# Optimization experiments

Measured on AMD Instinct MI355X. Metric: run time of the kernel, lower is better.

Reference implementation:

```python
import jax, jax.numpy as jnp
import numpy as np

NUM_EMBEDDINGS = 1024
EMBEDDING_DIM = 256
COMMITMENT_COST = 0.25


def setup_inputs() -> dict:
    key = jax.random.key(0)
    k_z, k_e = jax.random.split(key)
    z = jax.random.normal(k_z, (4, EMBEDDING_DIM, 16, 32, 32), dtype=jnp.float32)
    # torch init: uniform_(-1/K, 1/K)
    emb = jax.random.uniform(
        k_e, (NUM_EMBEDDINGS, EMBEDDING_DIM), dtype=jnp.float32,
        minval=-1.0 / NUM_EMBEDDINGS, maxval=1.0 / NUM_EMBEDDINGS)
    return {"z": z, "emb": emb}


def reference(z, emb):
    sg = jax.lax.stop_gradient
    b, c, d, h, w = z.shape
    K = emb.shape[0]
    # (B,C,D,H,W) -> (N, C)
    z_flat = jnp.transpose(z, (0, 2, 3, 4, 1)).reshape(-1, c)
    x_sq = jnp.sum(z_flat * z_flat, axis=1, keepdims=True)          # (N,1)
    e_sq = jnp.sum(emb * emb, axis=1)                                # (K,)
    xe = z_flat @ emb.T                                              # (N,K)
    distances = x_sq + e_sq[None, :] - 2.0 * xe
    encoding_indices = jnp.argmin(distances, axis=1)                 # (N,)
    z_q = emb[encoding_indices].reshape(b, d, h, w, c).transpose(0, 4, 1, 2, 3)
    embedding_loss = jnp.mean((sg(z_q) - z) ** 2)
    commitment_loss = COMMITMENT_COST * jnp.mean((z_q - sg(z)) ** 2)
    vq_loss = embedding_loss + commitment_loss
    z_q_st = z + sg(z_q - z)  # straight-through
    # perplexity from codebook usage histogram (== mean of one-hot encodings)
    counts = jnp.zeros((K,), z_flat.dtype).at[encoding_indices].add(1.0)
    avg_probs = counts / z_flat.shape[0]
    perplexity = jnp.exp(-jnp.sum(avg_probs * jnp.log(avg_probs + 1e-10)))
    return z_q_st, vq_loss, perplexity, encoding_indices.reshape(b, d, h, w)
```

## Files before the change

kernel.cpp:

```cpp
#include <hip/hip_runtime.h>


#define C_DIM 256
#define K_CODES 1024
#define N_VEC 65536
#define T_GAP 4e-4f

#define OUT_ZQ_SIZE 16777216
#define OUT_LOSS_OFF 16777216
#define OUT_PP_OFF   16777217
#define OUT_IDX_OFF  16777218

#define WS_EH    0
#define WS_EL    524288
#define WS_ESQ   1048576
#define WS_XSQ   1052672
#define WS_CNT   1314816
#define WS_LOSS  1318912
#define WS_FLC   1318920
#define WS_SIDX  1318928
#define WS_FLIST 1581072
#define WS_PM1   1843264
#define WS_EMBT  1843264
#define WS_PM2   2891840
#define WS_PIX   3940416

typedef __attribute__((ext_vector_type(8))) short short8;
typedef __attribute__((ext_vector_type(8))) unsigned short ushort8;
typedef __attribute__((ext_vector_type(16))) float f32x16;

__device__ __forceinline__ unsigned short bf16_rne(float v) {
    unsigned u = __float_as_uint(v);
    unsigned r = (u + 0x7FFFu + ((u >> 16) & 1u)) >> 16;
    return (unsigned short)r;
}



__global__ __launch_bounds__(256) void convert_z_kernel(const float* __restrict__ z,
                                                        unsigned short* __restrict__ zhF,
                                                        unsigned short* __restrict__ zlF) {
    const int tid = threadIdx.x;
    const int ln = tid & 63;
    const int og = tid >> 6;
    const int n0 = blockIdx.x * 64;
    const int b = n0 >> 14, s0 = n0 & 16383;
    const int n = n0 + ln;
    const size_t zbase = ((size_t)b << 22) + s0 + ln;
    const size_t tbase = (size_t)(n >> 5) * 8192;
    const int lr = n & 31;
#pragma unroll
    for (int t = 0; t < 8; ++t) {
        int o = og + t * 4;
        int c0 = o * 8;
        ushort8 hb, lb;
#pragma unroll
        for (int j = 0; j < 8; ++j) {
            float v = z[zbase + ((size_t)(c0 + j) << 14)];
            unsigned short h = bf16_rne(v);
            hb[j] = h;
            lb[j] = bf16_rne(v - __uint_as_float((unsigned)h << 16));
        }
        size_t off = tbase + (size_t)(o >> 1) * 512 + (size_t)(lr + 32 * (o & 1)) * 8;
        *reinterpret_cast<ushort8*>(zhF + off) = hb;
        *reinterpret_cast<ushort8*>(zlF + off) = lb;
    }
}

__global__ __launch_bounds__(256) void convert_e_kernel(const float* __restrict__ emb,
                                                        unsigned short* __restrict__ ehF,
                                                        unsigned short* __restrict__ elF) {
    int t = blockIdx.x * 256 + threadIdx.x;
    int k = t >> 5, o = t & 31;
    int c0 = o * 8;
    ushort8 hb, lb;
#pragma unroll
    for (int j = 0; j < 8; ++j) {
        float v = emb[k * C_DIM + c0 + j];
        unsigned short h = bf16_rne(v);
        hb[j] = h;
        lb[j] = bf16_rne(v - __uint_as_float((unsigned)h << 16));
    }
    size_t off = (size_t)(k >> 5) * 8192 + (size_t)(o >> 1) * 512 + (size_t)((k & 31) + 32 * (o & 1)) * 8;
    *reinterpret_cast<ushort8*>(ehF + off) = hb;
    *reinterpret_cast<ushort8*>(elF + off) = lb;
}


__device__ __forceinline__ float pairwise_sq_128(const float* p) {
#pragma clang fp contract(off)
    float r[8];
#pragma unroll
    for (int j = 0; j < 8; ++j) { float v = p[j]; r[j] = v * v; }
#pragma unroll
    for (int i = 8; i < 128; i += 8)
#pragma unroll
        for (int j = 0; j < 8; ++j) { float v = p[i + j]; float t = v * v; r[j] = r[j] + t; }
    return ((r[0] + r[1]) + (r[2] + r[3])) + ((r[4] + r[5]) + (r[6] + r[7]));
}

__global__ __launch_bounds__(256) void esq_kernel(const float* __restrict__ emb,
                                                  float* __restrict__ esq) {
#pragma clang fp contract(off)
    __shared__ float tile[64 * 260];
    const int tid = threadIdx.x;
    const int k0 = blockIdx.x * 64;
#pragma unroll
    for (int r = 0; r < 64; ++r) {
        int idx = r * 256 + tid;
        tile[(idx >> 8) * 260 + (idx & 255)] = emb[k0 * C_DIM + idx];
    }
    __syncthreads();
    if (tid < 64) {
        const float* row = &tile[tid * 260];
        esq[k0 + tid] = pairwise_sq_128(row) + pairwise_sq_128(row + 128);
    }
}

__global__ __launch_bounds__(256) void xsq_kernel(const float* __restrict__ z,
                                                  float* __restrict__ xsq) {
#pragma clang fp contract(off)
    const int n = blockIdx.x * 256 + threadIdx.x;
    const int b = n >> 14, s = n & 16383;
    const float* base = z + ((size_t)b << 22) + s;
    float r[8], res;
#pragma unroll
    for (int j = 0; j < 8; ++j) { float v = base[(size_t)j << 14]; r[j] = v * v; }
#pragma unroll
    for (int i = 8; i < 128; i += 8)
#pragma unroll
        for (int j = 0; j < 8; ++j) { float v = base[(size_t)(i + j) << 14]; float t = v * v; r[j] = r[j] + t; }
    res = ((r[0] + r[1]) + (r[2] + r[3])) + ((r[4] + r[5]) + (r[6] + r[7]));
#pragma unroll
    for (int j = 0; j < 8; ++j) { float v = base[(size_t)(128 + j) << 14]; r[j] = v * v; }
#pragma unroll
    for (int i = 136; i < 256; i += 8)
#pragma unroll
        for (int j = 0; j < 8; ++j) { float v = base[(size_t)(i + j) << 14]; float t = v * v; r[j] = r[j] + t; }
    res = res + (((r[0] + r[1]) + (r[2] + r[3])) + ((r[4] + r[5]) + (r[6] + r[7])));
    xsq[n] = res;
}

__global__ __launch_bounds__(256) void transpose_kernel(const float* __restrict__ emb,
                                                        float* __restrict__ embT) {
    __shared__ float t[64][65];
    const int k0 = blockIdx.x * 64;
    const int c0 = blockIdx.y * 64;
    const int tx = threadIdx.x & 63, ty = threadIdx.x >> 6;
    for (int r = ty; r < 64; r += 4)
        t[r][tx] = emb[(k0 + r) * C_DIM + c0 + tx];
    __syncthreads();
    for (int r = ty; r < 64; r += 4)
        embT[(c0 + r) * K_CODES + k0 + tx] = t[tx][r];
}


__global__ __launch_bounds__(512, 1) void screen_kernel(
    const unsigned short* __restrict__ zhF, const unsigned short* __restrict__ zlF,
    const unsigned short* __restrict__ ehF, const unsigned short* __restrict__ elF,
    const float* __restrict__ esq, const float* __restrict__ xsq,
    float* __restrict__ pm1, float* __restrict__ pm2,
    unsigned short* __restrict__ pix) {
    __shared__ __align__(16) unsigned short abuf[2][64 * 512];
    __shared__ float xbuf[512];
    __shared__ float sm1[8][64], sm2[8][64];
    __shared__ int   si[8][64];

    const int tid = threadIdx.x;
    const int w = tid >> 6, l = tid & 63, lr = l & 31, lh = l >> 5;
    const int bid = blockIdx.x;
    const int v = (bid & 7) * 64 + (bid >> 3);
    const int nb = v >> 2, kb = v & 3;
    const int n0 = nb * 512;
    const int kw = kb * 256 + w * 32;
    const int loff = l * 8;

    short8 Eh[16], El[16];
    {
        const unsigned short* bh = ehF + (size_t)(kb * 8 + w) * 8192 + loff;
        const unsigned short* bl = elF + (size_t)(kb * 8 + w) * 8192 + loff;
#pragma unroll
        for (int q = 0; q < 16; ++q) {
            Eh[q] = *reinterpret_cast<const short8*>(bh + q * 512);
            El[q] = *reinterpret_cast<const short8*>(bl + q * 512);
        }
    }
    float esql[16];
#pragma unroll
    for (int r = 0; r < 16; ++r)
        esql[r] = esq[kw + (r & 3) + 8 * (r >> 2) + 4 * lh];

    __builtin_amdgcn_global_load_lds(
        (const __attribute__((address_space(1))) void*)(xsq + n0 + w * 64 + l),
        (__attribute__((address_space(3))) void*)&xbuf[w * 64], 4, 0, 0);

    asm volatile("s_waitcnt vmcnt(0)" ::: "memory");
    __builtin_amdgcn_s_barrier();

#define STAGE(S) do {                                                                   \
    const int _b = (S) & 1;                                                             \
    _Pragma("unroll")                                                                   \
    for (int ci = 0; ci < 8; ++ci) {                                                    \
        int c = 8 * w + ci;                                                             \
        const unsigned short* src = ((c & 32) ? zlF : zhF)                              \
            + (size_t)((n0 >> 5) + (S) * 2 + ((c >> 4) & 1)) * 8192                     \
            + (size_t)(c & 15) * 512 + loff;                                            \
        __builtin_amdgcn_global_load_lds(                                               \
            (const __attribute__((address_space(1))) void*)src,                         \
            (__attribute__((address_space(3))) void*)&abuf[_b][c * 512], 16, 0, 0);     \
    }                                                                                   \
} while (0)

    STAGE(0);

    float rm1 = 3.4e38f, rm2 = 3.4e38f;
    int   ri1 = 0;

    for (int s = 0; s < 8; ++s) {
        const int cur = s & 1;
        asm volatile("s_waitcnt vmcnt(0)" ::: "memory");
        __builtin_amdgcn_s_barrier();
        __builtin_amdgcn_sched_barrier(0);
        if (s < 7) STAGE(s + 1);

        f32x16 acc0, acc1;
#pragma unroll
        for (int r = 0; r < 16; ++r) { acc0[r] = 0.0f; acc1[r] = 0.0f; }

        __builtin_amdgcn_s_setprio(1);
#pragma unroll
        for (int q = 0; q < 16; ++q) {
            short8 azh0 = *reinterpret_cast<const short8*>(&abuf[cur][(q)      * 512 + loff]);
            short8 azh1 = *reinterpret_cast<const short8*>(&abuf[cur][(16 + q) * 512 + loff]);
            short8 azl0 = *reinterpret_cast<const short8*>(&abuf[cur][(32 + q) * 512 + loff]);
            short8 azl1 = *reinterpret_cast<const short8*>(&abuf[cur][(48 + q) * 512 + loff]);
            acc0 = __builtin_amdgcn_mfma_f32_32x32x16_bf16(Eh[q], azh0, acc0, 0, 0, 0);
            acc1 = __builtin_amdgcn_mfma_f32_32x32x16_bf16(Eh[q], azh1, acc1, 0, 0, 0);
            acc0 = __builtin_amdgcn_mfma_f32_32x32x16_bf16(Eh[q], azl0, acc0, 0, 0, 0);
            acc1 = __builtin_amdgcn_mfma_f32_32x32x16_bf16(Eh[q], azl1, acc1, 0, 0, 0);
            acc0 = __builtin_amdgcn_mfma_f32_32x32x16_bf16(El[q], azh0, acc0, 0, 0, 0);
            acc1 = __builtin_amdgcn_mfma_f32_32x32x16_bf16(El[q], azh1, acc1, 0, 0, 0);
        }
        __builtin_amdgcn_s_setprio(0);

#pragma unroll
        for (int i = 0; i < 2; ++i) {
            const f32x16 a = i ? acc1 : acc0;
            const float xs = xbuf[s * 64 + i * 32 + lr];
            float m1 = 3.4e38f, m2 = 3.4e38f;
            int i1 = 0;
#pragma unroll
            for (int r = 0; r < 16; ++r) {
                float sv = (xs + esql[r]) - 2.0f * a[r];
                int kg = kw + (r & 3) + 8 * (r >> 2) + 4 * lh;
                if (sv < m1) { m2 = m1; m1 = sv; i1 = kg; }
                else m2 = fminf(m2, sv);
            }
            float om1 = __shfl_xor(m1, 32, 64);
            float om2 = __shfl_xor(m2, 32, 64);
            int   oi  = __shfl_xor(i1, 32, 64);
            if (om1 < m1)      { m2 = fminf(m1, om2); m1 = om1; i1 = oi; }
            else if (om1 > m1) { m2 = fminf(m2, om1); }
            else               { m2 = m1; i1 = min(i1, oi); }
            if (lh == 0) { sm1[w][i * 32 + lr] = m1; sm2[w][i * 32 + lr] = m2; si[w][i * 32 + lr] = i1; }
        }
        asm volatile("s_waitcnt lgkmcnt(0)" ::: "memory");
        __builtin_amdgcn_s_barrier();
        __builtin_amdgcn_sched_barrier(0);

        if (w == s) {
            float m1 = sm1[0][l], m2 = sm2[0][l];
            int i1 = si[0][l];
#pragma unroll
            for (int ww = 1; ww < 8; ++ww) {
                float q1 = sm1[ww][l], q2 = sm2[ww][l];
                int qi = si[ww][l];
                if (q1 < m1)      { m2 = fminf(m1, q2); m1 = q1; i1 = qi; }
                else if (q1 > m1) { m2 = fminf(m2, q1); }
                else              { m2 = m1; }
            }
            rm1 = m1; rm2 = m2; ri1 = i1;
        }
    }
#undef STAGE

    {
        size_t p = (size_t)kb * N_VEC + n0 + w * 64 + l;
        pm1[p] = rm1; pm2[p] = rm2; pix[p] = (unsigned short)ri1;
    }
}

__global__ __launch_bounds__(256) void merge_kernel(
    const float* __restrict__ pm1, const float* __restrict__ pm2,
    const unsigned short* __restrict__ pix,
    int* __restrict__ screen_idx, unsigned* __restrict__ flag_list,
    unsigned* __restrict__ flag_count) {
    int n = blockIdx.x * 256 + threadIdx.x;
    float m1 = 3.4e38f, m2 = 3.4e38f;
    int i1 = 0;
    for (int kb = 0; kb < 4; ++kb) {
        size_t p = (size_t)kb * N_VEC + n;
        float a1 = pm1[p], a2 = pm2[p];
        int ai = (int)pix[p];
        if (a1 < m1)      { m2 = fminf(m1, a2); m1 = a1; i1 = ai; }
        else if (a1 > m1) { m2 = fminf(m2, a1); }
        else              { m2 = m1; i1 = min(i1, ai); }
    }
    if (m2 - m1 <= T_GAP) {
        screen_idx[n] = -1;
        unsigned pos = atomicAdd(flag_count, 1u);
        flag_list[pos] = (unsigned)n;
    } else {
        screen_idx[n] = i1;
    }
}


__global__ __launch_bounds__(256) void refine_kernel(
    const float* __restrict__ z, const float* __restrict__ embT,
    const float* __restrict__ esq, const float* __restrict__ xsq,
    const unsigned* __restrict__ flag_list, const unsigned* __restrict__ flag_count,
    float* __restrict__ out_idx, unsigned* __restrict__ counts) {
#pragma clang fp contract(off)
    __shared__ float zrow[8][256];
    __shared__ int nrow[8];
    __shared__ unsigned long long red[8][4];
    const int tid = threadIdx.x;
    const unsigned cnt = *flag_count;
    const unsigned groups = (cnt + 7) >> 3;
    const int kbase = tid * 4;
    for (unsigned g = blockIdx.x; g < groups; g += gridDim.x) {
        __syncthreads();
        if (tid < 8) nrow[tid] = (g * 8 + tid < cnt) ? (int)flag_list[g * 8 + tid] : -1;
        __syncthreads();
        for (int r = 0; r < 8; ++r) {
            int n = nrow[r];
            if (n >= 0) {
                int b = n >> 14, s = n & 16383;
                zrow[r][tid] = z[((size_t)b << 22) + ((size_t)tid << 14) + s];
            }
        }
        __syncthreads();
        float acc[8][4];
#pragma unroll
        for (int r = 0; r < 8; ++r)
#pragma unroll
            for (int j = 0; j < 4; ++j) acc[r][j] = 0.0f;
        for (int c4 = 0; c4 < 64; ++c4) {
            float4 ek[4];
#pragma unroll
            for (int x = 0; x < 4; ++x)
                ek[x] = *reinterpret_cast<const float4*>(embT + (size_t)(c4 * 4 + x) * K_CODES + kbase);
#pragma unroll
            for (int r = 0; r < 8; ++r) {
                float4 zv = *reinterpret_cast<const float4*>(&zrow[r][c4 * 4]);
                float a;
                a = acc[r][0];
                a = fmaf(zv.x, ek[0].x, a); a = fmaf(zv.y, ek[1].x, a);
                a = fmaf(zv.z, ek[2].x, a); a = fmaf(zv.w, ek[3].x, a);
                acc[r][0] = a;
                a = acc[r][1];
                a = fmaf(zv.x, ek[0].y, a); a = fmaf(zv.y, ek[1].y, a);
                a = fmaf(zv.z, ek[2].y, a); a = fmaf(zv.w, ek[3].y, a);
                acc[r][1] = a;
                a = acc[r][2];
                a = fmaf(zv.x, ek[0].z, a); a = fmaf(zv.y, ek[1].z, a);
                a = fmaf(zv.z, ek[2].z, a); a = fmaf(zv.w, ek[3].z, a);
                acc[r][2] = a;
                a = acc[r][3];
                a = fmaf(zv.x, ek[0].w, a); a = fmaf(zv.y, ek[1].w, a);
                a = fmaf(zv.z, ek[2].w, a); a = fmaf(zv.w, ek[3].w, a);
                acc[r][3] = a;
            }
        }
        float esql[4];
#pragma unroll
        for (int j = 0; j < 4; ++j) esql[j] = esq[kbase + j];
#pragma unroll
        for (int r = 0; r < 8; ++r) {
            int n = nrow[r];
            float xs = (n >= 0) ? xsq[n] : 0.0f;
            float m = 3.4e38f;
            int mi = 0;
#pragma unroll
            for (int j = 0; j < 4; ++j) {
                float t1 = xs + esql[j];
                float d = t1 - 2.0f * acc[r][j];
                if (d < m) { m = d; mi = kbase + j; }
            }
            unsigned long long p = ((unsigned long long)__float_as_uint(m) << 32) | (unsigned)mi;
            for (int off = 32; off >= 1; off >>= 1) {
                unsigned long long o = __shfl_xor(p, off, 64);
                p = (o < p) ? o : p;
            }
            if ((tid & 63) == 0) red[r][tid >> 6] = p;
        }
        __syncthreads();
        if (tid < 8 && nrow[tid] >= 0) {
            unsigned long long p = red[tid][0];
#pragma unroll
            for (int ww = 1; ww < 4; ++ww) { unsigned long long o = red[tid][ww]; p = (o < p) ? o : p; }
            int idx = (int)(p & 0xFFFFFFFFull);
            out_idx[nrow[tid]] = (float)idx;
            atomicAdd(&counts[idx], 1u);
        }
    }
}

__global__ __launch_bounds__(256) void emit_kernel(const int* __restrict__ screen_idx,
                                                   float* __restrict__ out_idx,
                                                   unsigned* __restrict__ counts) {
    int n = blockIdx.x * 256 + threadIdx.x;
    int iv = screen_idx[n];
    if (iv >= 0) {
        out_idx[n] = (float)iv;
        atomicAdd(&counts[iv], 1u);
    }
}


__global__ __launch_bounds__(256) void gather_kernel(
    const float* __restrict__ z, const float* __restrict__ embT,
    const float* __restrict__ out_idx, float* __restrict__ out,
    double* __restrict__ loss_acc) {
    const int tid = threadIdx.x;
    const int ct = blockIdx.x & 3;
    const int st = (blockIdx.x >> 2) & 15;
    const int b  = blockIdx.x >> 6;
    const int s0 = st * 1024;
    const int c0 = ct * 64;

    int idx[4];
#pragma unroll
    for (int q = 0; q < 4; ++q)
        idx[q] = (int)out_idx[(b << 14) + s0 + 4 * tid + q];

    const float* zb = z + ((size_t)b << 22) + s0 + 4 * tid;
    float* ob = out + ((size_t)b << 22) + s0 + 4 * tid;

    double local = 0.0;
    for (int c = 0; c < 64; ++c) {
        const int cg = c0 + c;
        const float* er = embT + (size_t)cg * K_CODES;
        float4 zv = *reinterpret_cast<const float4*>(zb + ((size_t)cg << 14));
        float4 ov;
        float d0 = er[idx[0]] - zv.x;
        float d1 = er[idx[1]] - zv.y;
        float d2 = er[idx[2]] - zv.z;
        float d3 = er[idx[3]] - zv.w;
        ov.x = zv.x + d0; ov.y = zv.y + d1; ov.z = zv.z + d2; ov.w = zv.w + d3;
        *reinterpret_cast<float4*>(ob + ((size_t)cg << 14)) = ov;
        local += (double)d0 * d0 + (double)d1 * d1 + (double)d2 * d2 + (double)d3 * d3;
    }
    for (int off = 32; off >= 1; off >>= 1) local += __shfl_down(local, off, 64);
    __shared__ double redd[4];
    if ((tid & 63) == 0) redd[tid >> 6] = local;
    __syncthreads();
    if (tid == 0) atomicAdd(loss_acc, redd[0] + redd[1] + redd[2] + redd[3]);
}

__global__ void finalize_kernel(const unsigned* __restrict__ counts,
                                const double* __restrict__ loss_acc,
                                float* __restrict__ out) {
    int tid = threadIdx.x;
    double s = 0.0;
    for (int k = tid; k < K_CODES; k += 256) {
        float avg = (float)counts[k] / 65536.0f;
        float t = avg * logf(avg + 1e-10f);
        s += (double)t;
    }
    for (int off = 32; off >= 1; off >>= 1) s += __shfl_down(s, off, 64);
    __shared__ double red[4];
    if ((tid & 63) == 0) red[tid >> 6] = s;
    __syncthreads();
    if (tid == 0) {
        double tot = red[0] + red[1] + red[2] + red[3];
        out[OUT_PP_OFF]   = expf((float)(-tot));
        out[OUT_LOSS_OFF] = 1.25f * (float)(loss_acc[0] / 16777216.0);
    }
}

extern "C" void kernel_launch(void* const* d_in, const int* in_sizes, int n_in,
                              void* d_out, int out_size, void* d_ws, size_t ws_size,
                              hipStream_t stream) {
    const float* z   = (const float*)d_in[0];
    const float* emb = (const float*)d_in[1];
    float* out = (float*)d_out;
    char* ws = (char*)d_ws;

    unsigned short* ehF = (unsigned short*)(ws + WS_EH);
    unsigned short* elF = (unsigned short*)(ws + WS_EL);
    float*    esq       = (float*)(ws + WS_ESQ);
    float*    xsq       = (float*)(ws + WS_XSQ);
    unsigned* counts    = (unsigned*)(ws + WS_CNT);
    double*   loss_acc  = (double*)(ws + WS_LOSS);
    unsigned* flag_cnt  = (unsigned*)(ws + WS_FLC);
    int*      sidx      = (int*)(ws + WS_SIDX);
    unsigned* flist     = (unsigned*)(ws + WS_FLIST);
    float*    pm1       = (float*)(ws + WS_PM1);
    float*    pm2       = (float*)(ws + WS_PM2);
    unsigned short* pix = (unsigned short*)(ws + WS_PIX);
    float*    embT      = (float*)(ws + WS_EMBT);

    unsigned short* zhF = (unsigned short*)out;
    unsigned short* zlF = (unsigned short*)(out + 8388608);
    float* out_idx = out + OUT_IDX_OFF;

    hipMemsetAsync(ws + WS_CNT, 0, 4108, stream);

    convert_z_kernel<<<1024, 256, 0, stream>>>(z, zhF, zlF);
    convert_e_kernel<<<128, 256, 0, stream>>>(emb, ehF, elF);
    esq_kernel<<<K_CODES / 64, 256, 0, stream>>>(emb, esq);
    xsq_kernel<<<N_VEC / 256, 256, 0, stream>>>(z, xsq);
    screen_kernel<<<512, 512, 0, stream>>>(zhF, zlF, ehF, elF, esq, xsq, pm1, pm2, pix);
    merge_kernel<<<256, 256, 0, stream>>>(pm1, pm2, pix, sidx, flist, flag_cnt);
    transpose_kernel<<<dim3(16, 4), 256, 0, stream>>>(emb, embT);
    refine_kernel<<<1024, 256, 0, stream>>>(z, embT, esq, xsq, flist, flag_cnt, out_idx, counts);
    emit_kernel<<<256, 256, 0, stream>>>(sidx, out_idx, counts);
    gather_kernel<<<256, 256, 0, stream>>>(z, embT, out_idx, out, loss_acc);
    finalize_kernel<<<1, 256, 0, stream>>>(counts, loss_acc, out);
}
```

Baseline: 276.6 us.

## Fuse norm computations into conversion kernels and remove a barrier per screen stage

Computes the per-vector squared norms inside the z conversion kernel, using an LDS-staged tile, and the codebook norms inside the embedding conversion kernel. This drops two separate kernels and a second full read of z. The screen kernel double-buffers its per-wave partial minima so that each stage's cross-wave reduction is deferred to the next stage, removing one barrier per iteration. The merge kernel now writes indices and counts directly, which eliminates the emit kernel and the screen_idx buffer. A stray label was added inside the unrolled loop.

```diff
diff --git a/kernel.cpp b/kernel.cpp
--- a/kernel.cpp
+++ b/kernel.cpp
@@ -18,7 +18,6 @@
 #define WS_CNT   1314816
 #define WS_LOSS  1318912
 #define WS_FLC   1318920
-#define WS_SIDX  1318928
 #define WS_FLIST 1581072
 #define WS_PM1   1843264
 #define WS_EMBT  1843264
@@ -39,37 +38,75 @@
 
 __global__ __launch_bounds__(256) void convert_z_kernel(const float* __restrict__ z,
                                                         unsigned short* __restrict__ zhF,
-                                                        unsigned short* __restrict__ zlF) {
+                                                        unsigned short* __restrict__ zlF,
+                                                        float* __restrict__ xsq) {
+#pragma clang fp contract(off)
+    __shared__ float tile[128][65];
     const int tid = threadIdx.x;
     const int ln = tid & 63;
     const int og = tid >> 6;
     const int n0 = blockIdx.x * 64;
     const int b = n0 >> 14, s0 = n0 & 16383;
     const int n = n0 + ln;
-    const size_t zbase = ((size_t)b << 22) + s0 + ln;
     const size_t tbase = (size_t)(n >> 5) * 8192;
     const int lr = n & 31;
-#pragma unroll
-    for (int t = 0; t < 8; ++t) {
-        int o = og + t * 4;
-        int c0 = o * 8;
-        ushort8 hb, lb;
-#pragma unroll
-        for (int j = 0; j < 8; ++j) {
-            float v = z[zbase + ((size_t)(c0 + j) << 14)];
-            unsigned short h = bf16_rne(v);
-            hb[j] = h;
-            lb[j] = bf16_rne(v - __uint_as_float((unsigned)h << 16));
-        }
-        size_t off = tbase + (size_t)(o >> 1) * 512 + (size_t)(lr + 32 * (o & 1)) * 8;
-        *reinterpret_cast<ushort8*>(zhF + off) = hb;
-        *reinterpret_cast<ushort8*>(zlF + off) = lb;
-    }
+    float res = 0.0f;
+
+    for (int p = 0; p < 2; ++p) {
+        __syncthreads();
+        for (int i = 0; i < 32; ++i) {
+            int c = p * 128 + i * 4 + og;
+            tile[i * 4 + og][ln] = z[((size_t)b << 22) + ((size_t)c << 14) + s0 + ln];
+        }
+        __syncthreads();
+#pragma unroll
+        for (int t = 0; t < 4; ++t) {
+            int oh = og + t * 4;
+            int o  = p * 16 + oh;
+            ushort8 hb, lb;
+#pragma unroll
+            for (int j = 0; j < 8; ++j) {
+                float v = tile[oh * 8 + j][ln];
+                unsigned short h = bf16_rne(v);
+                hb[j] = h;
+                lb[j] = bf16_rne(v - __uint_as_float((unsigned)h << 16));
+            }
+            size_t off = tbase + (size_t)(o >> 1) * 512 + (size_t)(lr + 32 * (o & 1)) * 8;
+            *reinterpret_cast<ushort8*>(zhF + off) = hb;
+            *reinterpret_cast<ushort8*>(zlF + off) = lb;
+        }
+        if (tid < 64) {
+            float r[8];
+#pragma unroll
+            for (int j = 0; j < 8; ++j) { float v = tile[j][tid]; r[j] = v * v; }
+#pragma unroll
+            for (int i = 8; i < 128; i += 8)
+#pragma unroll
+                for (int j = 0; j < 8; ++j) { float v = tile[i + j][tid]; float t2 = v * v; r[j] = r[j] + t2; }
+            float blk = ((r[0] + r[1]) + (r[2] + r[3])) + ((r[4] + r[5]) + (r[6] + r[7]));
+            res = (p == 0) ? blk : res + blk;
+        }
+    }
+    if (tid < 64) xsq[n0 + tid] = res;
+}
+
+__device__ __forceinline__ float pairwise_sq_128(const float* p) {
+#pragma clang fp contract(off)
+    float r[8];
+#pragma unroll
+    for (int j = 0; j < 8; ++j) { float v = p[j]; r[j] = v * v; }
+#pragma unroll
+    for (int i = 8; i < 128; i += 8)
+#pragma unroll
+        for (int j = 0; j < 8; ++j) { float v = p[i + j]; float t = v * v; r[j] = r[j] + t; }
+    return ((r[0] + r[1]) + (r[2] + r[3])) + ((r[4] + r[5]) + (r[6] + r[7]));
 }
 
 __global__ __launch_bounds__(256) void convert_e_kernel(const float* __restrict__ emb,
                                                         unsigned short* __restrict__ ehF,
-                                                        unsigned short* __restrict__ elF) {
+                                                        unsigned short* __restrict__ elF,
+                                                        float* __restrict__ esq) {
+#pragma clang fp contract(off)
     int t = blockIdx.x * 256 + threadIdx.x;
     int k = t >> 5, o = t & 31;
     int c0 = o * 8;
@@ -84,61 +121,11 @@
     size_t off = (size_t)(k >> 5) * 8192 + (size_t)(o >> 1) * 512 + (size_t)((k & 31) + 32 * (o & 1)) * 8;
     *reinterpret_cast<ushort8*>(ehF + off) = hb;
     *reinterpret_cast<ushort8*>(elF + off) = lb;
-}
-
-
-__device__ __forceinline__ float pairwise_sq_128(const float* p) {
-#pragma clang fp contract(off)
-    float r[8];
-#pragma unroll
-    for (int j = 0; j < 8; ++j) { float v = p[j]; r[j] = v * v; }
-#pragma unroll
-    for (int i = 8; i < 128; i += 8)
-#pragma unroll
-        for (int j = 0; j < 8; ++j) { float v = p[i + j]; float t = v * v; r[j] = r[j] + t; }
-    return ((r[0] + r[1]) + (r[2] + r[3])) + ((r[4] + r[5]) + (r[6] + r[7]));
-}
-
-__global__ __launch_bounds__(256) void esq_kernel(const float* __restrict__ emb,
-                                                  float* __restrict__ esq) {
-#pragma clang fp contract(off)
-    __shared__ float tile[64 * 260];
-    const int tid = threadIdx.x;
-    const int k0 = blockIdx.x * 64;
-#pragma unroll
-    for (int r = 0; r < 64; ++r) {
-        int idx = r * 256 + tid;
-        tile[(idx >> 8) * 260 + (idx & 255)] = emb[k0 * C_DIM + idx];
-    }
-    __syncthreads();
-    if (tid < 64) {
-        const float* row = &tile[tid * 260];
-        esq[k0 + tid] = pairwise_sq_128(row) + pairwise_sq_128(row + 128);
-    }
-}
-
-__global__ __launch_bounds__(256) void xsq_kernel(const float* __restrict__ z,
-                                                  float* __restrict__ xsq) {
-#pragma clang fp contract(off)
-    const int n = blockIdx.x * 256 + threadIdx.x;
-    const int b = n >> 14, s = n & 16383;
-    const float* base = z + ((size_t)b << 22) + s;
-    float r[8], res;
-#pragma unroll
-    for (int j = 0; j < 8; ++j) { float v = base[(size_t)j << 14]; r[j] = v * v; }
-#pragma unroll
-    for (int i = 8; i < 128; i += 8)
-#pragma unroll
-        for (int j = 0; j < 8; ++j) { float v = base[(size_t)(i + j) << 14]; float t = v * v; r[j] = r[j] + t; }
-    res = ((r[0] + r[1]) + (r[2] + r[3])) + ((r[4] + r[5]) + (r[6] + r[7]));
-#pragma unroll
-    for (int j = 0; j < 8; ++j) { float v = base[(size_t)(128 + j) << 14]; r[j] = v * v; }
-#pragma unroll
-    for (int i = 136; i < 256; i += 8)
-#pragma unroll
-        for (int j = 0; j < 8; ++j) { float v = base[(size_t)(i + j) << 14]; float t = v * v; r[j] = r[j] + t; }
-    res = res + (((r[0] + r[1]) + (r[2] + r[3])) + ((r[4] + r[5]) + (r[6] + r[7])));
-    xsq[n] = res;
+    if (threadIdx.x < 8) {
+        int k8 = blockIdx.x * 8 + threadIdx.x;
+        const float* row = emb + (size_t)k8 * C_DIM;
+        esq[k8] = pairwise_sq_128(row) + pairwise_sq_128(row + 128);
+    }
 }
 
 __global__ __launch_bounds__(256) void transpose_kernel(const float* __restrict__ emb,
@@ -163,8 +150,8 @@
     unsigned short* __restrict__ pix) {
     __shared__ __align__(16) unsigned short abuf[2][64 * 512];
     __shared__ float xbuf[512];
-    __shared__ float sm1[8][64], sm2[8][64];
-    __shared__ int   si[8][64];
+    __shared__ float smp1[2][8][64], smp2[2][8][64];
+    __shared__ int   smi[2][8][64];
 
     const int tid = threadIdx.x;
     const int w = tid >> 6, l = tid & 63, lr = l & 31, lh = l >> 5;
@@ -182,6 +169,7 @@
 #pragma unroll
         for (int q = 0; q < 16; ++q) {
             Eh[q] = *reinterpret_cast<const short8*>(bh + q * 512);
+            Bl_dummy:;
             El[q] = *reinterpret_cast<const short8*>(bl + q * 512);
         }
     }
@@ -218,10 +206,25 @@
 
     for (int s = 0; s < 8; ++s) {
         const int cur = s & 1;
-        asm volatile("s_waitcnt vmcnt(0)" ::: "memory");
+        asm volatile("s_waitcnt vmcnt(0) lgkmcnt(0)" ::: "memory");
         __builtin_amdgcn_s_barrier();
         __builtin_amdgcn_sched_barrier(0);
         if (s < 7) STAGE(s + 1);
+
+        if (s >= 1 && w == s - 1) {
+            const int pp = (s - 1) & 1;
+            float m1 = smp1[pp][0][l], m2 = smp2[pp][0][l];
+            int i1 = smi[pp][0][l];
+#pragma unroll
+            for (int ww = 1; ww < 8; ++ww) {
+                float q1 = smp1[pp][ww][l], q2 = smp2[pp][ww][l];
+                int qi = smi[pp][ww][l];
+                if (q1 < m1)      { m2 = fminf(m1, q2); m1 = q1; i1 = qi; }
+                else if (q1 > m1) { m2 = fminf(m2, q1); }
+                else              { m2 = m1; }
+            }
+            rm1 = m1; rm2 = m2; ri1 = i1;
+        }
 
         f32x16 acc0, acc1;
 #pragma unroll
@@ -262,27 +265,30 @@
             if (om1 < m1)      { m2 = fminf(m1, om2); m1 = om1; i1 = oi; }
             else if (om1 > m1) { m2 = fminf(m2, om1); }
             else               { m2 = m1; i1 = min(i1, oi); }
-            if (lh == 0) { sm1[w][i * 32 + lr] = m1; sm2[w][i * 32 + lr] = m2; si[w][i * 32 + lr] = i1; }
-        }
-        asm volatile("s_waitcnt lgkmcnt(0)" ::: "memory");
-        __builtin_amdgcn_s_barrier();
-        __builtin_amdgcn_sched_barrier(0);
-
-        if (w == s) {
-            float m1 = sm1[0][l], m2 = sm2[0][l];
-            int i1 = si[0][l];
-#pragma unroll
-            for (int ww = 1; ww < 8; ++ww) {
-                float q1 = sm1[ww][l], q2 = sm2[ww][l];
-                int qi = si[ww][l];
-                if (q1 < m1)      { m2 = fminf(m1, q2); m1 = q1; i1 = qi; }
-                else if (q1 > m1) { m2 = fminf(m2, q1); }
-                else              { m2 = m1; }
-            }
-            rm1 = m1; rm2 = m2; ri1 = i1;
+            if (lh == 0) {
+                smp1[s & 1][w][i * 32 + lr] = m1;
+                smp2[s & 1][w][i * 32 + lr] = m2;
+                smi [s & 1][w][i * 32 + lr] = i1;
+            }
         }
     }
 #undef STAGE
+
+    asm volatile("s_waitcnt lgkmcnt(0)" ::: "memory");
+    __builtin_amdgcn_s_barrier();
+    if (w == 7) {
+        float m1 = smp1[1][0][l], m2 = smp2[1][0][l];
+        int i1 = smi[1][0][l];
+#pragma unroll
+        for (int ww = 1; ww < 8; ++ww) {
+            float q1 = smp1[1][ww][l], q2 = smp2[1][ww][l];
+            int qi = smi[1][ww][l];
+            if (q1 < m1)      { m2 = fminf(m1, q2); m1 = q1; i1 = qi; }
+            else if (q1 > m1) { m2 = fminf(m2, q1); }
+            else              { m2 = m1; }
+        }
+        rm1 = m1; rm2 = m2; ri1 = i1;
+    }
 
     {
         size_t p = (size_t)kb * N_VEC + n0 + w * 64 + l;
@@ -293,8 +299,8 @@
 __global__ __launch_bounds__(256) void merge_kernel(
     const float* __restrict__ pm1, const float* __restrict__ pm2,
     const unsigned short* __restrict__ pix,
-    int* __restrict__ screen_idx, unsigned* __restrict__ flag_list,
-    unsigned* __restrict__ flag_count) {
+    unsigned* __restrict__ flag_list, unsigned* __restrict__ flag_count,
+    float* __restrict__ out_idx, unsigned* __restrict__ counts) {
     int n = blockIdx.x * 256 + threadIdx.x;
     float m1 = 3.4e38f, m2 = 3.4e38f;
     int i1 = 0;
@@ -307,11 +313,11 @@
         else              { m2 = m1; i1 = min(i1, ai); }
     }
     if (m2 - m1 <= T_GAP) {
-        screen_idx[n] = -1;
         unsigned pos = atomicAdd(flag_count, 1u);
         flag_list[pos] = (unsigned)n;
     } else {
-        screen_idx[n] = i1;
+        out_idx[n] = (float)i1;
+        atomicAdd(&counts[i1], 1u);
     }
 }
 
@@ -407,17 +413,6 @@
     }
 }
 
-__global__ __launch_bounds__(256) void emit_kernel(const int* __restrict__ screen_idx,
-                                                   float* __restrict__ out_idx,
-                                                   unsigned* __restrict__ counts) {
-    int n = blockIdx.x * 256 + threadIdx.x;
-    int iv = screen_idx[n];
-    if (iv >= 0) {
-        out_idx[n] = (float)iv;
-        atomicAdd(&counts[iv], 1u);
-    }
-}
-
 
 __global__ __launch_bounds__(256) void gather_kernel(
     const float* __restrict__ z, const float* __restrict__ embT,
@@ -495,7 +490,6 @@
     unsigned* counts    = (unsigned*)(ws + WS_CNT);
     double*   loss_acc  = (double*)(ws + WS_LOSS);
     unsigned* flag_cnt  = (unsigned*)(ws + WS_FLC);
-    int*      sidx      = (int*)(ws + WS_SIDX);
     unsigned* flist     = (unsigned*)(ws + WS_FLIST);
     float*    pm1       = (float*)(ws + WS_PM1);
     float*    pm2       = (float*)(ws + WS_PM2);
@@ -508,15 +502,12 @@
 
     hipMemsetAsync(ws + WS_CNT, 0, 4108, stream);
 
-    convert_z_kernel<<<1024, 256, 0, stream>>>(z, zhF, zlF);
-    convert_e_kernel<<<128, 256, 0, stream>>>(emb, ehF, elF);
-    esq_kernel<<<K_CODES / 64, 256, 0, stream>>>(emb, esq);
-    xsq_kernel<<<N_VEC / 256, 256, 0, stream>>>(z, xsq);
+    convert_z_kernel<<<1024, 256, 0, stream>>>(z, zhF, zlF, xsq);
+    convert_e_kernel<<<128, 256, 0, stream>>>(emb, ehF, elF, esq);
     screen_kernel<<<512, 512, 0, stream>>>(zhF, zlF, ehF, elF, esq, xsq, pm1, pm2, pix);
-    merge_kernel<<<256, 256, 0, stream>>>(pm1, pm2, pix, sidx, flist, flag_cnt);
+    merge_kernel<<<256, 256, 0, stream>>>(pm1, pm2, pix, flist, flag_cnt, out_idx, counts);
     transpose_kernel<<<dim3(16, 4), 256, 0, stream>>>(emb, embT);
     refine_kernel<<<1024, 256, 0, stream>>>(z, embT, esq, xsq, flist, flag_cnt, out_idx, counts);
-    emit_kernel<<<256, 256, 0, stream>>>(sidx, out_idx, counts);
     gather_kernel<<<256, 256, 0, stream>>>(z, embT, out_idx, out, loss_acc);
     finalize_kernel<<<1, 256, 0, stream>>>(counts, loss_acc, out);
 }
```

Result: faster. 245.0 us (-11.4%).
